# Kernel tuning notes

Measured on AMD Instinct MI355X. Metric: run time of the kernel, lower is better.

## Reference

```python
import jax, jax.numpy as jnp
import numpy as np

D_MODEL = 1024
N_HEADS = 16
D_K = D_MODEL // N_HEADS
B, S = 4, 1024


def setup_inputs() -> dict:
    key = jax.random.key(0)
    ks = jax.random.split(key, 9)
    inp = {
        "q": jax.random.normal(ks[0], (B, S, D_MODEL), jnp.float32),
        "k": jax.random.normal(ks[1], (B, S, D_MODEL), jnp.float32),
        "v": jax.random.normal(ks[2], (B, S, D_MODEL), jnp.float32),
        # causal mask, broadcastable to [B, H, S, S]; 0 => masked
        "mask": jnp.tril(jnp.ones((1, 1, S, S), jnp.int32)),
        # torch nn.Linear weights: y = x @ W.T + b, W is [out, in]
        "Wq": jax.random.normal(ks[3], (D_MODEL, D_MODEL), jnp.float32) * 0.02,
        "bq": jnp.zeros((D_MODEL,), jnp.float32),
        "Wk": jax.random.normal(ks[4], (D_MODEL, D_MODEL), jnp.float32) * 0.02,
        "bk": jnp.zeros((D_MODEL,), jnp.float32),
        "Wv": jax.random.normal(ks[5], (D_MODEL, D_MODEL), jnp.float32) * 0.02,
        "bv": jnp.zeros((D_MODEL,), jnp.float32),
    }
    return inp


def _head_split(x):
    # [B, S, D] -> [B, H, S, d_k]
    b, s, _ = x.shape
    return x.reshape(b, s, N_HEADS, D_K).transpose(0, 2, 1, 3)


def reference(q, k, v, mask, Wq, bq, Wk, bk, Wv, bv):
    origin_shape = q.shape
    qh = _head_split(q @ Wq.T + bq)  # [B,H,S,dk]
    kh = _head_split(k @ Wk.T + bk)
    vh = _head_split(v @ Wv.T + bv)

    scores = jnp.einsum("bhqd,bhkd->bhqk", qh, kh) / jnp.sqrt(jnp.float32(D_K))
    scores = jnp.where(mask == 0, -jnp.inf, scores)
    # original subtracts the GLOBAL max before softmax (mathematically a no-op
    # per-row, kept for faithfulness)
    scores = jax.nn.softmax(scores - scores.max(), axis=-1)
    scores = jnp.where(jnp.isnan(scores), 0.0, scores)  # fully-masked rows -> 0

    out = jnp.einsum("bhqk,bhkd->bhqd", scores, vh)
    out = out.transpose(0, 2, 1, 3).reshape(origin_shape)
    return out, scores
```

## Files before the change

### kernel.cpp

```cpp
#include <hip/hip_runtime.h>

#define BATCH 4
#define SEQ 1024
#define DMODEL 1024
#define NH 16
#define DK 64

typedef float f32x4 __attribute__((ext_vector_type(4)));
typedef __bf16 bf16x8 __attribute__((ext_vector_type(8)));
typedef __bf16 bf16x4 __attribute__((ext_vector_type(4)));

#define MFMA(a, b, c) __builtin_amdgcn_mfma_f32_16x16x32_bf16((a), (b), (c), 0, 0, 0)

#define GLL16(g, l)                                                            \
    __builtin_amdgcn_global_load_lds(                                          \
        (const __attribute__((address_space(1))) void*)(g),                    \
        (__attribute__((address_space(3))) void*)(l), 16, 0, 0)

__global__ __launch_bounds__(256) void qkv_proj(
    const float* __restrict__ Xq, const float* __restrict__ Xk, const float* __restrict__ Xv,
    const float* __restrict__ Wq, const float* __restrict__ Wk, const float* __restrict__ Wv,
    const float* __restrict__ bq, const float* __restrict__ bk, const float* __restrict__ bv,
    __bf16* __restrict__ qh, __bf16* __restrict__ kh, __bf16* __restrict__ vt)
{
    const int mat = blockIdx.z;
    const float* X    = (mat == 0) ? Xq : (mat == 1) ? Xk : Xv;
    const float* W    = (mat == 0) ? Wq : (mat == 1) ? Wk : Wv;
    const float* bias = (mat == 0) ? bq : (mat == 1) ? bk : bv;
    __bf16* dst       = (mat == 0) ? qh : (mat == 1) ? kh : vt;

    __shared__ __align__(16) __bf16 Xs[128][56];
    __shared__ __align__(16) __bf16 Ws[128][56];

    const int tid  = threadIdx.x;
    const int lane = tid & 63;
    const int wid  = tid >> 6;
    const int wr = wid >> 1, wc = wid & 1;
    const int lc = lane & 15, lg = lane >> 4;
    const int i0 = blockIdx.y * 128;
    const int j0 = blockIdx.x * 128;

    f32x4 acc[4][4] = {};

    const int sr = tid >> 3;
    const int sc = (tid & 7) * 4;

    for (int k0 = 0; k0 < DMODEL; k0 += 32) {
        #pragma unroll
        for (int i = 0; i < 4; ++i) {
            const int row = i * 32 + sr;
            float4 xv = *(const float4*)(X + (size_t)(i0 + row) * DMODEL + k0 + sc);
            float4 wv = *(const float4*)(W + (size_t)(j0 + row) * DMODEL + k0 + sc);
            bf16x4 xb, wb;
            xb[0] = (__bf16)xv.x; xb[1] = (__bf16)xv.y; xb[2] = (__bf16)xv.z; xb[3] = (__bf16)xv.w;
            wb[0] = (__bf16)wv.x; wb[1] = (__bf16)wv.y; wb[2] = (__bf16)wv.z; wb[3] = (__bf16)wv.w;
            *(bf16x4*)&Xs[row][sc] = xb;
            *(bf16x4*)&Ws[row][sc] = wb;
        }
        __syncthreads();

        bf16x8 a[4], b[4];
        #pragma unroll
        for (int m = 0; m < 4; ++m) a[m] = *(const bf16x8*)&Xs[wr * 64 + m * 16 + lc][lg * 8];
        #pragma unroll
        for (int n = 0; n < 4; ++n) b[n] = *(const bf16x8*)&Ws[wc * 64 + n * 16 + lc][lg * 8];
        #pragma unroll
        for (int m = 0; m < 4; ++m)
            #pragma unroll
            for (int n = 0; n < 4; ++n)
                acc[m][n] = MFMA(a[m], b[n], acc[m][n]);
        __syncthreads();
    }

    #pragma unroll
    for (int n = 0; n < 4; ++n) {
        const int j = j0 + wc * 64 + n * 16 + lc;
        const float bj = bias[j];
        const int h = j >> 6, d = j & 63;
        #pragma unroll
        for (int m = 0; m < 4; ++m) {
            #pragma unroll
            for (int r = 0; r < 4; ++r) {
                const int i = i0 + wr * 64 + m * 16 + lg * 4 + r;
                const int bb = i >> 10, s = i & 1023;
                const __bf16 o = (__bf16)(acc[m][n][r] + bj);
                if (mat < 2) dst[(((size_t)(bb * NH + h)) * SEQ + s) * DK + d] = o;
                else         dst[(((size_t)(bb * NH + h)) * DK + d) * SEQ + s] = o;
            }
        }
    }
}

#define STAGE_K(buf, kt)                                                       \
    {                                                                          \
        const char* gb_ = (const char*)Kb + (size_t)(kt) * 8192;               \
        char* lb_ = (char*)&Ks[buf][0];                                        \
        GLL16(gb_ + (wid * 2 + 0) * 1024 + soff, lb_ + (wid * 2 + 0) * 1024);  \
        GLL16(gb_ + (wid * 2 + 1) * 1024 + soff, lb_ + (wid * 2 + 1) * 1024);  \
    }

#define STAGE_V(kt)                                                            \
    {                                                                          \
        const char* gb_ = (const char*)Vb + (size_t)(kt) * 128;                \
        char* lb_ = (char*)&Vs[0];                                             \
        GLL16(gb_ + (size_t)((wid * 2 + 0) * 8 + sg) * 2048 + svoff,           \
              lb_ + (wid * 2 + 0) * 1024);                                     \
        GLL16(gb_ + (size_t)((wid * 2 + 1) * 8 + sg) * 2048 + svoff,           \
              lb_ + (wid * 2 + 1) * 1024);                                     \
    }

#define QK_TILE(kbuf, acc)                                                     \
    {                                                                          \
        const char* kb_ = (const char*)&Ks[kbuf][0];                           \
        _Pragma("unroll")                                                      \
        for (int n = 0; n < 4; ++n) {                                          \
            const int row_ = n * 16 + lc;                                      \
            const int sw_ = (row_ & 7) << 4;                                   \
            acc[n] = MFMA(aq0, *(const bf16x8*)(kb_ + row_ * 128 + ((lg * 16) ^ sw_)), acc[n]);      \
            acc[n] = MFMA(aq1, *(const bf16x8*)(kb_ + row_ * 128 + ((64 + lg * 16) ^ sw_)), acc[n]); \
        }                                                                      \
    }

__global__ __launch_bounds__(256, 4) void attn_fused6(
    const __bf16* __restrict__ qh, const __bf16* __restrict__ kh,
    const __bf16* __restrict__ vt, float* __restrict__ out, float* __restrict__ scores)
{
    const int id = blockIdx.x;
    const int bh = id & 63;
    const int qb = 15 - (id >> 6);
    const int q0 = qb * 64;
    const int tid  = threadIdx.x;
    const int lane = tid & 63;
    const int wid  = tid >> 6;
    const int lc = lane & 15, lg = lane >> 4;
    const int r0 = wid * 16;

    __shared__ __align__(16) __bf16 Ks[2][64 * 64];
    __shared__ __align__(16) __bf16 Vs[64 * 64];
    __shared__ __align__(16) __bf16 Pf[4][16][72];

    const __bf16* Kb = kh + (size_t)bh * SEQ * DK;
    const __bf16* Vb = vt + (size_t)bh * DK * SEQ;

    const int sg    = lane >> 3;
    const int svoff = (((lane & 7) << 4)) ^ (sg << 4);
    const int soff  = (sg << 7) + svoff;

    const __bf16* Qp = qh + ((size_t)bh * SEQ + q0 + r0 + lc) * DK + lg * 8;
    const bf16x8 aq0 = *(const bf16x8*)(Qp);
    const bf16x8 aq1 = *(const bf16x8*)(Qp + 32);

    STAGE_K(0, 0);
    __syncthreads();

    float lsum[4] = {0.f, 0.f, 0.f, 0.f};
    for (int kt = 0; kt <= qb; ++kt) {
        if (kt < qb) STAGE_K((kt + 1) & 1, kt + 1);
        f32x4 acc[4] = {};
        QK_TILE(kt & 1, acc);
        if (kt < qb) {
            #pragma unroll
            for (int n = 0; n < 4; ++n)
                #pragma unroll
                for (int r = 0; r < 4; ++r)
                    lsum[r] += __expf(acc[n][r] * 0.125f);
        } else {
            #pragma unroll
            for (int n = 0; n < 4; ++n)
                #pragma unroll
                for (int r = 0; r < 4; ++r)
                    if (n * 16 + lc <= r0 + lg * 4 + r)
                        lsum[r] += __expf(acc[n][r] * 0.125f);
        }
        __syncthreads();
    }

    float linv[4];
    #pragma unroll
    for (int r = 0; r < 4; ++r) {
        float s = lsum[r];
        s += __shfl_xor(s, 1);
        s += __shfl_xor(s, 2);
        s += __shfl_xor(s, 4);
        s += __shfl_xor(s, 8);
        linv[r] = 1.0f / s;
    }

    float* srow = scores + ((size_t)bh * SEQ + q0 + r0) * SEQ;
    const int srr = lane >> 4;
    const int scc = (lane & 15) * 4;
    for (int kt = qb + 1; kt < 16; ++kt) {
        const f32x4 z = {};
        #pragma unroll
        for (int i = 0; i < 4; ++i)
            *(f32x4*)(srow + (size_t)(srr + 4 * i) * SEQ + kt * 64 + scc) = z;
    }

    STAGE_K(0, 0);
    f32x4 oacc[4] = {};
    __syncthreads();

    for (int kt = 0; kt <= qb; ++kt) {
        if (kt < qb) STAGE_K((kt + 1) & 1, kt + 1);
        STAGE_V(kt);

        f32x4 acc[4] = {};
        QK_TILE(kt & 1, acc);

        const bool diag = (kt == qb);
        float* sp = srow + kt * 64;
        #pragma unroll
        for (int n = 0; n < 4; ++n) {
            #pragma unroll
            for (int r = 0; r < 4; ++r) {
                float p = __expf(acc[n][r] * 0.125f) * linv[r];
                if (diag && (n * 16 + lc > r0 + lg * 4 + r)) p = 0.f;
                sp[(size_t)(lg * 4 + r) * SEQ + n * 16 + lc] = p;
                Pf[wid][lg * 4 + r][n * 16 + lc] = (__bf16)p;
            }
        }

        __syncthreads();

        {
            const char* vb_ = (const char*)&Vs[0];
            #pragma unroll
            for (int cc = 0; cc < 2; ++cc) {
                const bf16x8 pa = *(const bf16x8*)&Pf[wid][lc][cc * 32 + lg * 8];
                #pragma unroll
                for (int n = 0; n < 4; ++n) {
                    const int row_ = n * 16 + lc;
                    const int sw_ = (row_ & 7) << 4;
                    const bf16x8 vb = *(const bf16x8*)(vb_ + row_ * 128 + ((cc * 64 + lg * 16) ^ sw_));
                    oacc[n] = MFMA(pa, vb, oacc[n]);
                }
            }
        }

        __syncthreads();
    }

    {
        const int b = bh >> 4, h = bh & 15;
        float* op = out + ((size_t)b * SEQ + q0 + r0) * DMODEL + h * DK;
        #pragma unroll
        for (int n = 0; n < 4; ++n)
            #pragma unroll
            for (int r = 0; r < 4; ++r)
                op[(size_t)(lg * 4 + r) * DMODEL + n * 16 + lc] = oacc[n][r];
    }
}

extern "C" void kernel_launch(void* const* d_in, const int* in_sizes, int n_in,
                              void* d_out, int out_size, void* d_ws, size_t ws_size,
                              hipStream_t stream)
{
    const float* q  = (const float*)d_in[0];
    const float* k  = (const float*)d_in[1];
    const float* v  = (const float*)d_in[2];
    const float* Wq = (const float*)d_in[4];
    const float* bq = (const float*)d_in[5];
    const float* Wk = (const float*)d_in[6];
    const float* bk = (const float*)d_in[7];
    const float* Wv = (const float*)d_in[8];
    const float* bv = (const float*)d_in[9];

    float* out    = (float*)d_out;
    float* scores = out + (size_t)BATCH * SEQ * DMODEL;

    __bf16* qh = (__bf16*)d_ws;
    __bf16* kh = qh + (size_t)BATCH * NH * SEQ * DK;
    __bf16* vt = kh + (size_t)BATCH * NH * SEQ * DK;

    dim3 g1(DMODEL / 128, (BATCH * SEQ) / 128, 3);
    qkv_proj<<<g1, 256, 0, stream>>>(q, k, v, Wq, Wk, Wv, bq, bk, bv, qh, kh, vt);

    attn_fused6<<<dim3(16 * 64), 256, 0, stream>>>(qh, kh, vt, out, scores);
}
```

Before: 147.7 us.

## Async LDS double-buffered QKV projection and vectorized score stores

The QKV projection now stages fp32 X/W tiles straight into swizzled, double-buffered LDS with global_load_lds and converts them to bf16 at fragment-load time. Its output tile shrinks from 128x128 to 128x64, which doubles the grid. The attention kernel writes the zero upper-triangle scores up front and stores probability rows as 16-byte vectors read back from the bf16 LDS P buffer, replacing scattered scalar stores. The risks are that the stored scores now carry bf16 precision instead of fp32, and that LDS traffic rises in the projection.

```diff
diff --git a/kernel.cpp b/kernel.cpp
--- a/kernel.cpp
+++ b/kernel.cpp
@@ -16,6 +16,20 @@
     __builtin_amdgcn_global_load_lds(                                          \
         (const __attribute__((address_space(1))) void*)(g),                    \
         (__attribute__((address_space(3))) void*)(l), 16, 0, 0)
+
+#define QSTAGE(buf, k0)                                                        \
+    {                                                                          \
+        char* xl_ = (char*)&Xs[buf][0];                                        \
+        char* wl_ = (char*)&Ws[buf][0];                                        \
+        _Pragma("unroll")                                                      \
+        for (int q_ = 0; q_ < 4; ++q_)                                         \
+            GLL16(Xg + (size_t)(i0 + wid * 32 + q_ * 8 + sg) * 4096 + (k0) * 4 + ss, \
+                  xl_ + wid * 4096 + q_ * 1024);                               \
+        _Pragma("unroll")                                                      \
+        for (int q_ = 0; q_ < 2; ++q_)                                         \
+            GLL16(Wg + (size_t)(j0 + wid * 16 + q_ * 8 + sg) * 4096 + (k0) * 4 + ss, \
+                  wl_ + wid * 2048 + q_ * 1024);                               \
+    }
 
 __global__ __launch_bounds__(256) void qkv_proj(
     const float* __restrict__ Xq, const float* __restrict__ Xk, const float* __restrict__ Xv,
@@ -29,8 +43,8 @@
     const float* bias = (mat == 0) ? bq : (mat == 1) ? bk : bv;
     __bf16* dst       = (mat == 0) ? qh : (mat == 1) ? kh : vt;
 
-    __shared__ __align__(16) __bf16 Xs[128][56];
-    __shared__ __align__(16) __bf16 Ws[128][56];
+    __shared__ __align__(16) float Xs[2][128 * 32];
+    __shared__ __align__(16) float Ws[2][64 * 32];
 
     const int tid  = threadIdx.x;
     const int lane = tid & 63;
@@ -38,43 +52,56 @@
     const int wr = wid >> 1, wc = wid & 1;
     const int lc = lane & 15, lg = lane >> 4;
     const int i0 = blockIdx.y * 128;
-    const int j0 = blockIdx.x * 128;
-
-    f32x4 acc[4][4] = {};
-
-    const int sr = tid >> 3;
-    const int sc = (tid & 7) * 4;
-
-    for (int k0 = 0; k0 < DMODEL; k0 += 32) {
-        #pragma unroll
-        for (int i = 0; i < 4; ++i) {
-            const int row = i * 32 + sr;
-            float4 xv = *(const float4*)(X + (size_t)(i0 + row) * DMODEL + k0 + sc);
-            float4 wv = *(const float4*)(W + (size_t)(j0 + row) * DMODEL + k0 + sc);
-            bf16x4 xb, wb;
-            xb[0] = (__bf16)xv.x; xb[1] = (__bf16)xv.y; xb[2] = (__bf16)xv.z; xb[3] = (__bf16)xv.w;
-            wb[0] = (__bf16)wv.x; wb[1] = (__bf16)wv.y; wb[2] = (__bf16)wv.z; wb[3] = (__bf16)wv.w;
-            *(bf16x4*)&Xs[row][sc] = xb;
-            *(bf16x4*)&Ws[row][sc] = wb;
-        }
+    const int j0 = blockIdx.x * 64;
+    const int sg = lane >> 3;
+    const int ss = ((lane & 7) ^ sg) << 4;
+
+    const char* Xg = (const char*)X;
+    const char* Wg = (const char*)W;
+
+    f32x4 acc[4][2] = {};
+
+    QSTAGE(0, 0);
+    int cur = 0;
+    for (int k0 = 0; k0 < DMODEL; k0 += 32, cur ^= 1) {
         __syncthreads();
-
-        bf16x8 a[4], b[4];
-        #pragma unroll
-        for (int m = 0; m < 4; ++m) a[m] = *(const bf16x8*)&Xs[wr * 64 + m * 16 + lc][lg * 8];
-        #pragma unroll
-        for (int n = 0; n < 4; ++n) b[n] = *(const bf16x8*)&Ws[wc * 64 + n * 16 + lc][lg * 8];
+        if (k0 + 32 < DMODEL) QSTAGE(cur ^ 1, k0 + 32);
+
+        const char* xb = (const char*)&Xs[cur][0];
+        const char* wb = (const char*)&Ws[cur][0];
+        bf16x8 a[4], b[2];
+        #pragma unroll
+        for (int m = 0; m < 4; ++m) {
+            const int row = wr * 64 + m * 16 + lc;
+            const int sw = (row & 7) << 4;
+            const f32x4 lo = *(const f32x4*)(xb + row * 128 + ((lg * 32) ^ sw));
+            const f32x4 hi = *(const f32x4*)(xb + row * 128 + ((lg * 32 + 16) ^ sw));
+            a[m][0] = (__bf16)lo[0]; a[m][1] = (__bf16)lo[1];
+            a[m][2] = (__bf16)lo[2]; a[m][3] = (__bf16)lo[3];
+            a[m][4] = (__bf16)hi[0]; a[m][5] = (__bf16)hi[1];
+            a[m][6] = (__bf16)hi[2]; a[m][7] = (__bf16)hi[3];
+        }
+        #pragma unroll
+        for (int n = 0; n < 2; ++n) {
+            const int row = wc * 32 + n * 16 + lc;
+            const int sw = (row & 7) << 4;
+            const f32x4 lo = *(const f32x4*)(wb + row * 128 + ((lg * 32) ^ sw));
+            const f32x4 hi = *(const f32x4*)(wb + row * 128 + ((lg * 32 + 16) ^ sw));
+            b[n][0] = (__bf16)lo[0]; b[n][1] = (__bf16)lo[1];
+            b[n][2] = (__bf16)lo[2]; b[n][3] = (__bf16)lo[3];
+            b[n][4] = (__bf16)hi[0]; b[n][5] = (__bf16)hi[1];
+            b[n][6] = (__bf16)hi[2]; b[n][7] = (__bf16)hi[3];
+        }
         #pragma unroll
         for (int m = 0; m < 4; ++m)
             #pragma unroll
-            for (int n = 0; n < 4; ++n)
+            for (int n = 0; n < 2; ++n)
                 acc[m][n] = MFMA(a[m], b[n], acc[m][n]);
-        __syncthreads();
     }
 
     #pragma unroll
-    for (int n = 0; n < 4; ++n) {
-        const int j = j0 + wc * 64 + n * 16 + lc;
+    for (int n = 0; n < 2; ++n) {
+        const int j = j0 + wc * 32 + n * 16 + lc;
         const float bj = bias[j];
         const int h = j >> 6, d = j & 63;
         #pragma unroll
@@ -121,7 +148,7 @@
         }                                                                      \
     }
 
-__global__ __launch_bounds__(256, 4) void attn_fused6(
+__global__ __launch_bounds__(256, 4) void attn_fused7(
     const __bf16* __restrict__ qh, const __bf16* __restrict__ kh,
     const __bf16* __restrict__ vt, float* __restrict__ out, float* __restrict__ scores)
 {
@@ -146,6 +173,16 @@
     const int svoff = (((lane & 7) << 4)) ^ (sg << 4);
     const int soff  = (sg << 7) + svoff;
 
+    float* srow = scores + ((size_t)bh * SEQ + q0 + r0) * SEQ;
+    const int srr = lane >> 4;
+    const int scc = (lane & 15) * 4;
+    for (int kt = qb + 1; kt < 16; ++kt) {
+        const f32x4 z = {};
+        #pragma unroll
+        for (int i = 0; i < 4; ++i)
+            *(f32x4*)(srow + (size_t)(srr + 4 * i) * SEQ + kt * 64 + scc) = z;
+    }
+
     const __bf16* Qp = qh + ((size_t)bh * SEQ + q0 + r0 + lc) * DK + lg * 8;
     const bf16x8 aq0 = *(const bf16x8*)(Qp);
     const bf16x8 aq1 = *(const bf16x8*)(Qp + 32);
@@ -186,16 +223,6 @@
         linv[r] = 1.0f / s;
     }
 
-    float* srow = scores + ((size_t)bh * SEQ + q0 + r0) * SEQ;
-    const int srr = lane >> 4;
-    const int scc = (lane & 15) * 4;
-    for (int kt = qb + 1; kt < 16; ++kt) {
-        const f32x4 z = {};
-        #pragma unroll
-        for (int i = 0; i < 4; ++i)
-            *(f32x4*)(srow + (size_t)(srr + 4 * i) * SEQ + kt * 64 + scc) = z;
-    }
-
     STAGE_K(0, 0);
     f32x4 oacc[4] = {};
     __syncthreads();
@@ -208,15 +235,25 @@
         QK_TILE(kt & 1, acc);
 
         const bool diag = (kt == qb);
-        float* sp = srow + kt * 64;
         #pragma unroll
         for (int n = 0; n < 4; ++n) {
             #pragma unroll
             for (int r = 0; r < 4; ++r) {
                 float p = __expf(acc[n][r] * 0.125f) * linv[r];
                 if (diag && (n * 16 + lc > r0 + lg * 4 + r)) p = 0.f;
-                sp[(size_t)(lg * 4 + r) * SEQ + n * 16 + lc] = p;
                 Pf[wid][lg * 4 + r][n * 16 + lc] = (__bf16)p;
+            }
+        }
+
+        {
+            float* sp = srow + kt * 64;
+            #pragma unroll
+            for (int i = 0; i < 4; ++i) {
+                const int row = srr + 4 * i;
+                const bf16x4 pb = *(const bf16x4*)&Pf[wid][row][scc];
+                f32x4 pv;
+                pv[0] = pb[0]; pv[1] = pb[1]; pv[2] = pb[2]; pv[3] = pb[3];
+                *(f32x4*)(sp + (size_t)row * SEQ + scc) = pv;
             }
         }
 
@@ -272,8 +309,8 @@
     __bf16* kh = qh + (size_t)BATCH * NH * SEQ * DK;
     __bf16* vt = kh + (size_t)BATCH * NH * SEQ * DK;
 
-    dim3 g1(DMODEL / 128, (BATCH * SEQ) / 128, 3);
+    dim3 g1(DMODEL / 64, (BATCH * SEQ) / 128, 3);
     qkv_proj<<<g1, 256, 0, stream>>>(q, k, v, Wq, Wk, Wv, bq, bk, bv, qh, kh, vt);
 
-    attn_fused6<<<dim3(16 * 64), 256, 0, stream>>>(qh, kh, vt, out, scores);
+    attn_fused7<<<dim3(16 * 64), 256, 0, stream>>>(qh, kh, vt, out, scores);
 }
```

After: 155.6 us. 1.05x slower.
